# Performance work log

Hardware: AMD Instinct MI355X
Metric: run time of the kernel (lower is better)

## Reference

```python
import jax, jax.numpy as jnp
import numpy as np

M, K, N = 2048, 4096, 8192
BITS = 4
GROUP_SIZE = 128
G = K // GROUP_SIZE  # 32 groups
PACK = 8 // BITS     # 2 values per int8 byte


def setup_inputs() -> dict:
    key = jax.random.key(0)
    k_a, k_q, k_s = jax.random.split(key, 3)
    A = jax.random.normal(k_a, (M, K), dtype=jnp.float16)
    # packed 4-bit weights: each byte stores two uint4 values (low nibble first)
    qweight = jax.random.randint(k_q, (N, K // PACK), 0, 256, dtype=jnp.int32)
    scales = jax.random.normal(k_s, (N, G), dtype=jnp.float16)
    zeros = jnp.zeros((N, G), dtype=jnp.float16)
    bias = jnp.zeros((N,), dtype=jnp.float16)
    return {"A": A, "qweight": qweight, "scales": scales, "zeros": zeros, "bias": bias}


def _dequantize(qweight, scales, zeros):
    # unpack two uint4 values per byte (low nibble is the earlier element)
    q = qweight.astype(jnp.int32)
    lo = q & 0xF
    hi = (q >> 4) & 0xF
    intw = jnp.stack([lo, hi], axis=-1).reshape(N, K)  # [N, K] uint4 values
    # zeros_mode='original': w = (q - zero) * scale, per group of GROUP_SIZE
    wq = intw.reshape(N, G, GROUP_SIZE).astype(jnp.float16)
    w = (wq - zeros[:, :, None]) * scales[:, :, None]
    return w.reshape(N, K)


def reference(A, qweight, scales, zeros, bias):
    W = _dequantize(qweight, scales, zeros)          # [N, K] fp16
    out = jnp.einsum('mk,nk->mn', A, W) + bias       # 'nt' layout: A @ W^T + bias
    return out.astype(A.dtype)
```

## Files before the change

kernel.cpp:

```cpp
#include <hip/hip_runtime.h>
#include <stdint.h>

#define MDIM 2048
#define KDIM 4096
#define NDIM 8192
#define NG   32
#define QROW 2048
#define NT2  64
#define LSTR 36
#define BUFH 32768

typedef __attribute__((ext_vector_type(4))) float    f32x4;
typedef __attribute__((ext_vector_type(2))) _Float16 f16x2;
typedef __attribute__((ext_vector_type(8))) _Float16 f16x8;
typedef __attribute__((ext_vector_type(4))) int      i32x4;

#define CVT2(a,b) __builtin_bit_cast(f16x2, __builtin_amdgcn_cvt_pkrtz((a),(b)))
#define BCU(x)    __builtin_bit_cast(unsigned, (x))
#define BCH2(x)   __builtin_bit_cast(f16x2, (x))
#define MFMA16(A,B,C) __builtin_amdgcn_mfma_f32_16x16x32_f16((A),(B),(C),0,0,0)
#define LDSREAD(DST, OFF) __builtin_memcpy(&(DST), &lds[(OFF)], 16)

__device__ __forceinline__ void gload_lds16(const void* g, void* l) {
  __builtin_amdgcn_global_load_lds(
      (const __attribute__((address_space(1))) void*)g,
      (__attribute__((address_space(3))) void*)l, 16, 0, 0);
}

__device__ __forceinline__ uint4 dequant8(i32x4 q, float sf, float zf) {
  const _Float16 sh = (_Float16)sf;
  const _Float16 bh = (_Float16)(-zf * sf);
  const f16x2 s2 = {sh, sh}, b2 = {bh, bh};
  const f16x2 k2 = {(_Float16)1024.0f, (_Float16)1024.0f};
  uint4 r;
#define DQE(QV, DST) do {                                                   \
    unsigned Bb_ = (unsigned)(QV) & 0xFFu;                                  \
    unsigned bits_ = ((Bb_ | (Bb_ << 12)) & 0x000F000Fu) | 0x64006400u;     \
    DST = BCU((f16x2)((BCH2(bits_) - k2) * s2 + b2));                       \
  } while (0)
  DQE(q.x, r.x); DQE(q.y, r.y); DQE(q.z, r.z); DQE(q.w, r.w);
#undef DQE
  return r;
}

__global__ __launch_bounds__(256) void dequant_w_kernel(
    const int* __restrict__ qw, const float* __restrict__ scales,
    const float* __restrict__ zeros, _Float16* __restrict__ Wf)
{
  const size_t total = (size_t)NDIM * (KDIM / 8);
  for (size_t t = (size_t)blockIdx.x * blockDim.x + threadIdx.x; t < total;
       t += (size_t)gridDim.x * blockDim.x) {
    i32x4 q;
    __builtin_memcpy(&q, qw + 4 * t, 16);
    const int n = (int)(t >> 9);
    const int k = (int)((t & 511) << 3);
    const int g = k >> 7;
    uint4 w = dequant8(q, scales[n * NG + g], zeros[n * NG + g]);
    __builtin_memcpy(Wf + (size_t)n * KDIM + k, &w, 16);
  }
}

__global__ __launch_bounds__(256) void conv_a_kernel(
    const float* __restrict__ A, _Float16* __restrict__ Af)
{
  const size_t total = (size_t)MDIM * (KDIM / 8);
  for (size_t t = (size_t)blockIdx.x * blockDim.x + threadIdx.x; t < total;
       t += (size_t)gridDim.x * blockDim.x) {
    f32x4 v0, v1;
    __builtin_memcpy(&v0, A + 8 * t,     16);
    __builtin_memcpy(&v1, A + 8 * t + 4, 16);
    uint4 h;
    h.x = BCU(CVT2(v0.x, v0.y));
    h.y = BCU(CVT2(v0.z, v0.w));
    h.z = BCU(CVT2(v1.x, v1.y));
    h.w = BCU(CVT2(v1.z, v1.w));
    __builtin_memcpy(Af + 8 * t, &h, 16);
  }
}

__global__ __launch_bounds__(512) void gemm_f16_kernel(
    const _Float16* __restrict__ Af,
    const _Float16* __restrict__ Wf,
    const float* __restrict__ bias,
    float* __restrict__ out)
{
  __shared__ __align__(16) _Float16 lds[2 * BUFH];

  const int tid  = threadIdx.x;
  const int wave = tid >> 6;
  const int lane = tid & 63;
  const int n0 = blockIdx.x << 8;
  const int m0 = blockIdx.y << 8;
  const int wm = (wave >> 2) << 7;
  const int wn = (wave & 3) << 6;

  f32x4 acc[8][4] = {};

  const int srow   = tid >> 3;
  const int schunk = (tid & 7) ^ ((tid >> 3) & 7);
  const _Float16* aU0 = Af + (size_t)(m0 + srow) * KDIM + schunk * 8;
  const _Float16* aU1 = aU0 + (size_t)64 * KDIM;
  const _Float16* aU2 = aU0 + (size_t)128 * KDIM;
  const _Float16* aU3 = aU0 + (size_t)192 * KDIM;
  const _Float16* bU0 = Wf + (size_t)(n0 + srow) * KDIM + schunk * 8;
  const _Float16* bU1 = bU0 + (size_t)64 * KDIM;
  const _Float16* bU2 = bU0 + (size_t)128 * KDIM;
  const _Float16* bU3 = bU0 + (size_t)192 * KDIM;

#define ISSUE(T) do {                                                  \
    _Float16* d_ = &lds[((T) & 1) * BUFH + (wave << 9)];               \
    const size_t ko_ = (size_t)(T) << 6;                               \
    gload_lds16(aU0 + ko_, d_);                                        \
    gload_lds16(aU1 + ko_, d_ + 4096);                                 \
    gload_lds16(aU2 + ko_, d_ + 8192);                                 \
    gload_lds16(aU3 + ko_, d_ + 12288);                                \
    gload_lds16(bU0 + ko_, d_ + 16384);                                \
    gload_lds16(bU1 + ko_, d_ + 20480);                                \
    gload_lds16(bU2 + ko_, d_ + 24576);                                \
    gload_lds16(bU3 + ko_, d_ + 28672);                                \
  } while (0)

  const int fr = lane & 15;
  const int h4 = lane >> 4;
  const int ck0 = (((0 + h4) ^ (fr & 7))) << 3;
  const int ck1 = (((4 + h4) ^ (fr & 7))) << 3;
  int raOff[8], rbOff[4];
#pragma unroll
  for (int i = 0; i < 8; ++i) raOff[i] = (wm + 16 * i + fr) * 64;
#pragma unroll
  for (int j = 0; j < 4; ++j) rbOff[j] = 16384 + (wn + 16 * j + fr) * 64;

#define COMPUTE(T) do {                                                \
    const int bb_ = ((T) & 1) * BUFH;                                  \
    f16x8 b0_[4], b1_[4];                                              \
    _Pragma("unroll")                                                  \
    for (int j = 0; j < 4; ++j) {                                      \
      LDSREAD(b0_[j], bb_ + rbOff[j] + ck0);                           \
      LDSREAD(b1_[j], bb_ + rbOff[j] + ck1);                           \
    }                                                                  \
    _Pragma("unroll")                                                  \
    for (int i = 0; i < 8; ++i) {                                      \
      f16x8 a0_, a1_;                                                  \
      LDSREAD(a0_, bb_ + raOff[i] + ck0);                              \
      LDSREAD(a1_, bb_ + raOff[i] + ck1);                              \
      _Pragma("unroll")                                                \
      for (int j = 0; j < 4; ++j)                                      \
        acc[i][j] = MFMA16(a0_, b0_[j], acc[i][j]);                    \
      _Pragma("unroll")                                                \
      for (int j = 0; j < 4; ++j)                                      \
        acc[i][j] = MFMA16(a1_, b1_[j], acc[i][j]);                    \
    }                                                                  \
  } while (0)

#define PH_MFMA(R) do {                                                \
    __builtin_amdgcn_s_setprio(1);                                     \
    _Pragma("unroll")                                                  \
    for (int j = 0; j < 4; ++j) {                                      \
      acc[(R)][j]     = MFMA16(aA0, bf0[j], acc[(R)][j]);              \
      acc[(R) + 1][j] = MFMA16(aB0, bf0[j], acc[(R) + 1][j]);          \
    }                                                                  \
    _Pragma("unroll")                                                  \
    for (int j = 0; j < 4; ++j) {                                      \
      acc[(R)][j]     = MFMA16(aA1, bf1[j], acc[(R)][j]);              \
      acc[(R) + 1][j] = MFMA16(aB1, bf1[j], acc[(R) + 1][j]);          \
    }                                                                  \
    __builtin_amdgcn_s_setprio(0);                                     \
  } while (0)

  ISSUE(0); ISSUE(1);

#pragma clang loop unroll(disable)
  for (int t = 0; t < NT2 - 2; ++t) {
    asm volatile("s_waitcnt vmcnt(8)" ::: "memory");
    __builtin_amdgcn_s_barrier();
    const int bb = (t & 1) * BUFH;

    f16x8 bf0[4], bf1[4], aA0, aA1, aB0, aB1;

#pragma unroll
    for (int j = 0; j < 4; ++j) {
      LDSREAD(bf0[j], bb + rbOff[j] + ck0);
      LDSREAD(bf1[j], bb + rbOff[j] + ck1);
    }
    LDSREAD(aA0, bb + raOff[0] + ck0);
    LDSREAD(aA1, bb + raOff[0] + ck1);
    LDSREAD(aB0, bb + raOff[1] + ck0);
    LDSREAD(aB1, bb + raOff[1] + ck1);
    __builtin_amdgcn_s_barrier();
    PH_MFMA(0);

    LDSREAD(aA0, bb + raOff[2] + ck0);
    LDSREAD(aA1, bb + raOff[2] + ck1);
    LDSREAD(aB0, bb + raOff[3] + ck0);
    LDSREAD(aB1, bb + raOff[3] + ck1);
    __builtin_amdgcn_s_barrier();
    PH_MFMA(2);

    LDSREAD(aA0, bb + raOff[4] + ck0);
    LDSREAD(aA1, bb + raOff[4] + ck1);
    LDSREAD(aB0, bb + raOff[5] + ck0);
    LDSREAD(aB1, bb + raOff[5] + ck1);
    __builtin_amdgcn_s_barrier();
    PH_MFMA(4);

    LDSREAD(aA0, bb + raOff[6] + ck0);
    LDSREAD(aA1, bb + raOff[6] + ck1);
    LDSREAD(aB0, bb + raOff[7] + ck0);
    LDSREAD(aB1, bb + raOff[7] + ck1);
    __builtin_amdgcn_s_barrier();
    ISSUE(t + 2);
    PH_MFMA(6);
  }

  asm volatile("s_waitcnt vmcnt(8)" ::: "memory");
  __builtin_amdgcn_s_barrier();
  COMPUTE(NT2 - 2);
  asm volatile("s_waitcnt vmcnt(0)" ::: "memory");
  __builtin_amdgcn_s_barrier();
  COMPUTE(NT2 - 1);

#undef ISSUE
#undef COMPUTE
#undef PH_MFMA

  const int cr = (lane >> 4) << 2;
  const int cc = lane & 15;
#pragma unroll
  for (int j = 0; j < 4; ++j) {
    const int n = n0 + wn + j * 16 + cc;
    const float bv = bias[n];
#pragma unroll
    for (int i = 0; i < 8; ++i) {
      const int mrow = m0 + wm + i * 16 + cr;
#pragma unroll
      for (int r = 0; r < 4; ++r)
        out[(size_t)(mrow + r) * NDIM + n] = acc[i][j][r] + bv;
    }
  }
}

__global__ __launch_bounds__(256, 4) void qlin_fused_kernel(
    const float* __restrict__ A, const int* __restrict__ qw,
    const float* __restrict__ scales, const float* __restrict__ zeros,
    const float* __restrict__ bias, float* __restrict__ out)
{
  __shared__ _Float16 As[2][128 * LSTR];
  __shared__ _Float16 Bs[2][128 * LSTR];

  const int tid  = threadIdx.x;
  const int wave = tid >> 6;
  const int lane = tid & 63;
  const int n0 = blockIdx.x << 7;
  const int m0 = blockIdx.y << 7;
  const int wm = (wave >> 1) << 6;
  const int wn = (wave & 1) << 6;

  f32x4 acc[4][4] = {};

  const int r4 = tid >> 2;
  const int c4 = tid & 3;

  const float* aP0 = A + (size_t)(m0 + r4) * KDIM + c4 * 8;
  const float* aP1 = aP0 + (size_t)64 * KDIM;
  const int*   qP0 = qw + (size_t)(n0 + r4) * QROW + c4 * 4;
  const int*   qP1 = qP0 + (size_t)64 * QROW;
  const float* sP0 = scales + (size_t)(n0 + r4) * NG;
  const float* zP0 = zeros  + (size_t)(n0 + r4) * NG;
  const float* sP1 = sP0 + (size_t)64 * NG;
  const float* zP1 = zP0 + (size_t)64 * NG;

  const int aD0 = r4 * LSTR + c4 * 8;
  const int aD1 = (r4 + 64) * LSTR + c4 * 8;

  const int fr = lane & 15;
  const int k0 = (lane >> 4) * 8;
  const int ra0 = (wm +  0 + fr) * LSTR + k0;
  const int ra1 = (wm + 16 + fr) * LSTR + k0;
  const int ra2 = (wm + 32 + fr) * LSTR + k0;
  const int ra3 = (wm + 48 + fr) * LSTR + k0;
  const int rb0 = (wn +  0 + fr) * LSTR + k0;
  const int rb1 = (wn + 16 + fr) * LSTR + k0;
  const int rb2 = (wn + 32 + fr) * LSTR + k0;
  const int rb3 = (wn + 48 + fr) * LSTR + k0;

  f32x4 pa0, pa1, pa2, pa3;
  i32x4 pq0, pq1;
  float psf0, pzf0, psf1, pzf1;

#define ISSUE(KT) do {                                                        \
    __builtin_memcpy(&pa0, aP0 + (size_t)(KT) * 32,     16);                  \
    __builtin_memcpy(&pa1, aP0 + (size_t)(KT) * 32 + 4, 16);                  \
    __builtin_memcpy(&pa2, aP1 + (size_t)(KT) * 32,     16);                  \
    __builtin_memcpy(&pa3, aP1 + (size_t)(KT) * 32 + 4, 16);                  \
    __builtin_memcpy(&pq0, qP0 + (size_t)(KT) * 16, 16);                      \
    __builtin_memcpy(&pq1, qP1 + (size_t)(KT) * 16, 16);                      \
    const int g_ = (KT) >> 2;                                                 \
    psf0 = sP0[g_]; pzf0 = zP0[g_];                                           \
    psf1 = sP1[g_]; pzf1 = zP1[g_];                                           \
  } while (0)

#define STAGE(P) do {                                                         \
    uint4 aw0_;                                                               \
    aw0_.x = BCU(CVT2(pa0.x, pa0.y));                                         \
    aw0_.y = BCU(CVT2(pa0.z, pa0.w));                                         \
    aw0_.z = BCU(CVT2(pa1.x, pa1.y));                                         \
    aw0_.w = BCU(CVT2(pa1.z, pa1.w));                                         \
    __builtin_memcpy(&As[P][aD0], &aw0_, 16);                                 \
    uint4 aw1_;                                                               \
    aw1_.x = BCU(CVT2(pa2.x, pa2.y));                                         \
    aw1_.y = BCU(CVT2(pa2.z, pa2.w));                                         \
    aw1_.z = BCU(CVT2(pa3.x, pa3.y));                                         \
    aw1_.w = BCU(CVT2(pa3.z, pa3.w));                                         \
    __builtin_memcpy(&As[P][aD1], &aw1_, 16);                                 \
    uint4 bw0_ = dequant8(pq0, psf0, pzf0);                                   \
    __builtin_memcpy(&Bs[P][aD0], &bw0_, 16);                                 \
    uint4 bw1_ = dequant8(pq1, psf1, pzf1);                                   \
    __builtin_memcpy(&Bs[P][aD1], &bw1_, 16);                                 \
  } while (0)

#define COMPUTE(P) do {                                                       \
    f16x8 af[4], bfr[4];                                                      \
    __builtin_memcpy(&af[0], &As[P][ra0], 16);                                \
    __builtin_memcpy(&af[1], &As[P][ra1], 16);                                \
    __builtin_memcpy(&af[2], &As[P][ra2], 16);                                \
    __builtin_memcpy(&af[3], &As[P][ra3], 16);                                \
    __builtin_memcpy(&bfr[0], &Bs[P][rb0], 16);                               \
    __builtin_memcpy(&bfr[1], &Bs[P][rb1], 16);                               \
    __builtin_memcpy(&bfr[2], &Bs[P][rb2], 16);                               \
    __builtin_memcpy(&bfr[3], &Bs[P][rb3], 16);                               \
    _Pragma("unroll")                                                         \
    for (int i = 0; i < 4; ++i)                                               \
      _Pragma("unroll")                                                       \
      for (int j = 0; j < 4; ++j)                                             \
        acc[i][j] = MFMA16(af[i], bfr[j], acc[i][j]);                         \
  } while (0)

  ISSUE(0);
  STAGE(0);
  __syncthreads();

#pragma clang loop unroll(disable)
  for (int kt = 0; kt < 127; ++kt) {
    const int p = kt & 1;
    ISSUE(kt + 1);
    COMPUTE(p);
    STAGE(p ^ 1);
    __syncthreads();
  }
  COMPUTE(1);

#undef ISSUE
#undef STAGE
#undef COMPUTE

  const int cr = (lane >> 4) << 2;
  const int cc = lane & 15;
#pragma unroll
  for (int j = 0; j < 4; ++j) {
    const int n = n0 + wn + j * 16 + cc;
    const float bv = bias[n];
#pragma unroll
    for (int i = 0; i < 4; ++i) {
      const int mrow = m0 + wm + i * 16 + cr;
#pragma unroll
      for (int r = 0; r < 4; ++r)
        out[(size_t)(mrow + r) * NDIM + n] = acc[i][j][r] + bv;
    }
  }
}

extern "C" void kernel_launch(void* const* d_in, const int* in_sizes, int n_in,
                              void* d_out, int out_size, void* d_ws, size_t ws_size,
                              hipStream_t stream) {
  const float* A      = (const float*)d_in[0];
  const int*   qwp    = (const int*)d_in[1];
  const float* scales = (const float*)d_in[2];
  const float* zerosp = (const float*)d_in[3];
  const float* biasp  = (const float*)d_in[4];
  float*       outp   = (float*)d_out;

  const size_t needW = (size_t)NDIM * KDIM * sizeof(_Float16);
  const size_t needA = (size_t)MDIM * KDIM * sizeof(_Float16);

  if (ws_size >= needW + needA) {
    _Float16* Wf = (_Float16*)d_ws;
    _Float16* Af = (_Float16*)((char*)d_ws + needW);
    dequant_w_kernel<<<2048, 256, 0, stream>>>(qwp, scales, zerosp, Wf);
    conv_a_kernel<<<2048, 256, 0, stream>>>(A, Af);
    dim3 grid(NDIM / 256, MDIM / 256);
    gemm_f16_kernel<<<grid, 512, 0, stream>>>(Af, Wf, biasp, outp);
  } else {
    dim3 grid(NDIM / 128, MDIM / 128);
    qlin_fused_kernel<<<grid, 256, 0, stream>>>(A, qwp, scales, zerosp, biasp, outp);
  }
}
```

Before: 159.4 us.

## Switch f16 GEMM inner loop from 16x16x32 to 32x32x16 MFMA tiles

Replaces the 16x16x32 MFMA instructions with 32x32x16 MFMA, regrouping each wave's 128x64 tile into 4x2 blocks of 32x32 with 16-float accumulators. The LDS fragment reads, swizzled chunk offsets, phased barrier schedule and output store mapping are rewritten to match the new operand and accumulator layout. The larger instruction reuses each operand over more outputs, so fewer LDS reads and instructions are needed per FLOP. In exchange there are more K-steps per tile and a different pipeline phase balance with one A row block per phase.

```diff
diff --git a/kernel.cpp b/kernel.cpp
--- a/kernel.cpp
+++ b/kernel.cpp
@@ -10,15 +10,17 @@
 #define LSTR 36
 #define BUFH 32768
 
-typedef __attribute__((ext_vector_type(4))) float    f32x4;
-typedef __attribute__((ext_vector_type(2))) _Float16 f16x2;
-typedef __attribute__((ext_vector_type(8))) _Float16 f16x8;
-typedef __attribute__((ext_vector_type(4))) int      i32x4;
+typedef __attribute__((ext_vector_type(4)))  float    f32x4;
+typedef __attribute__((ext_vector_type(16))) float    f32x16;
+typedef __attribute__((ext_vector_type(2)))  _Float16 f16x2;
+typedef __attribute__((ext_vector_type(8)))  _Float16 f16x8;
+typedef __attribute__((ext_vector_type(4)))  int      i32x4;
 
 #define CVT2(a,b) __builtin_bit_cast(f16x2, __builtin_amdgcn_cvt_pkrtz((a),(b)))
 #define BCU(x)    __builtin_bit_cast(unsigned, (x))
 #define BCH2(x)   __builtin_bit_cast(f16x2, (x))
 #define MFMA16(A,B,C) __builtin_amdgcn_mfma_f32_16x16x32_f16((A),(B),(C),0,0,0)
+#define MFMA32(A,B,C) __builtin_amdgcn_mfma_f32_32x32x16_f16((A),(B),(C),0,0,0)
 #define LDSREAD(DST, OFF) __builtin_memcpy(&(DST), &lds[(OFF)], 16)
 
 __device__ __forceinline__ void gload_lds16(const void* g, void* l) {
@@ -94,7 +96,7 @@
   const int wm = (wave >> 2) << 7;
   const int wn = (wave & 3) << 6;
 
-  f32x4 acc[8][4] = {};
+  f32x16 acc[4][2] = {};
 
   const int srow   = tid >> 3;
   const int schunk = (tid & 7) ^ ((tid >> 3) & 7);
@@ -120,52 +122,55 @@
     gload_lds16(bU3 + ko_, d_ + 28672);                                \
   } while (0)
 
-  const int fr = lane & 15;
-  const int h4 = lane >> 4;
-  const int ck0 = (((0 + h4) ^ (fr & 7))) << 3;
-  const int ck1 = (((4 + h4) ^ (fr & 7))) << 3;
-  int raOff[8], rbOff[4];
-#pragma unroll
-  for (int i = 0; i < 8; ++i) raOff[i] = (wm + 16 * i + fr) * 64;
-#pragma unroll
-  for (int j = 0; j < 4; ++j) rbOff[j] = 16384 + (wn + 16 * j + fr) * 64;
+  const int fr32 = lane & 31;
+  const int h2   = lane >> 5;
+  const int sw8  = fr32 & 7;
+  int raOff[4], rbOff[2], ckk[4];
+#pragma unroll
+  for (int i = 0; i < 4; ++i) raOff[i] = (wm + 32 * i + fr32) * 64;
+#pragma unroll
+  for (int j = 0; j < 2; ++j) rbOff[j] = 16384 + (wn + 32 * j + fr32) * 64;
+#pragma unroll
+  for (int ks = 0; ks < 4; ++ks) ckk[ks] = ((2 * ks + h2) ^ sw8) << 3;
 
 #define COMPUTE(T) do {                                                \
     const int bb_ = ((T) & 1) * BUFH;                                  \
-    f16x8 b0_[4], b1_[4];                                              \
+    f16x8 b_[2][4];                                                    \
     _Pragma("unroll")                                                  \
-    for (int j = 0; j < 4; ++j) {                                      \
-      LDSREAD(b0_[j], bb_ + rbOff[j] + ck0);                           \
-      LDSREAD(b1_[j], bb_ + rbOff[j] + ck1);                           \
+    for (int j = 0; j < 2; ++j)                                        \
+      _Pragma("unroll")                                                \
+      for (int ks = 0; ks < 4; ++ks)                                   \
+        LDSREAD(b_[j][ks], bb_ + rbOff[j] + ckk[ks]);                  \
+    _Pragma("unroll")                                                  \
+    for (int i = 0; i < 4; ++i) {                                      \
+      _Pragma("unroll")                                                \
+      for (int ks = 0; ks < 4; ++ks) {                                 \
+        f16x8 a_;                                                      \
+        LDSREAD(a_, bb_ + raOff[i] + ckk[ks]);                         \
+        acc[i][0] = MFMA32(a_, b_[0][ks], acc[i][0]);                  \
+        acc[i][1] = MFMA32(a_, b_[1][ks], acc[i][1]);                  \
+      }                                                                \
     }                                                                  \
-    _Pragma("unroll")                                                  \
-    for (int i = 0; i < 8; ++i) {                                      \
-      f16x8 a0_, a1_;                                                  \
-      LDSREAD(a0_, bb_ + raOff[i] + ck0);                              \
-      LDSREAD(a1_, bb_ + raOff[i] + ck1);                              \
-      _Pragma("unroll")                                                \
-      for (int j = 0; j < 4; ++j)                                      \
-        acc[i][j] = MFMA16(a0_, b0_[j], acc[i][j]);                    \
-      _Pragma("unroll")                                                \
-      for (int j = 0; j < 4; ++j)                                      \
-        acc[i][j] = MFMA16(a1_, b1_[j], acc[i][j]);                    \
-    }                                                                  \
-  } while (0)
-
-#define PH_MFMA(R) do {                                                \
+  } while (0)
+
+#define PH_MFMA(I) do {                                                \
     __builtin_amdgcn_s_setprio(1);                                     \
-    _Pragma("unroll")                                                  \
-    for (int j = 0; j < 4; ++j) {                                      \
-      acc[(R)][j]     = MFMA16(aA0, bf0[j], acc[(R)][j]);              \
-      acc[(R) + 1][j] = MFMA16(aB0, bf0[j], acc[(R) + 1][j]);          \
-    }                                                                  \
-    _Pragma("unroll")                                                  \
-    for (int j = 0; j < 4; ++j) {                                      \
-      acc[(R)][j]     = MFMA16(aA1, bf1[j], acc[(R)][j]);              \
-      acc[(R) + 1][j] = MFMA16(aB1, bf1[j], acc[(R) + 1][j]);          \
-    }                                                                  \
+    acc[I][0] = MFMA32(aK0, bf[0][0], acc[I][0]);                      \
+    acc[I][1] = MFMA32(aK0, bf[1][0], acc[I][1]);                      \
+    acc[I][0] = MFMA32(aK1, bf[0][1], acc[I][0]);                      \
+    acc[I][1] = MFMA32(aK1, bf[1][1], acc[I][1]);                      \
+    acc[I][0] = MFMA32(aK2, bf[0][2], acc[I][0]);                      \
+    acc[I][1] = MFMA32(aK2, bf[1][2], acc[I][1]);                      \
+    acc[I][0] = MFMA32(aK3, bf[0][3], acc[I][0]);                      \
+    acc[I][1] = MFMA32(aK3, bf[1][3], acc[I][1]);                      \
     __builtin_amdgcn_s_setprio(0);                                     \
   } while (0)
+
+#define RD_A(I)                                                        \
+    LDSREAD(aK0, bb + raOff[I] + ckk[0]);                              \
+    LDSREAD(aK1, bb + raOff[I] + ckk[1]);                              \
+    LDSREAD(aK2, bb + raOff[I] + ckk[2]);                              \
+    LDSREAD(aK3, bb + raOff[I] + ckk[3]);
 
   ISSUE(0); ISSUE(1);
 
@@ -175,41 +180,29 @@
     __builtin_amdgcn_s_barrier();
     const int bb = (t & 1) * BUFH;
 
-    f16x8 bf0[4], bf1[4], aA0, aA1, aB0, aB1;
-
-#pragma unroll
-    for (int j = 0; j < 4; ++j) {
-      LDSREAD(bf0[j], bb + rbOff[j] + ck0);
-      LDSREAD(bf1[j], bb + rbOff[j] + ck1);
-    }
-    LDSREAD(aA0, bb + raOff[0] + ck0);
-    LDSREAD(aA1, bb + raOff[0] + ck1);
-    LDSREAD(aB0, bb + raOff[1] + ck0);
-    LDSREAD(aB1, bb + raOff[1] + ck1);
+    f16x8 bf[2][4], aK0, aK1, aK2, aK3;
+
+#pragma unroll
+    for (int j = 0; j < 2; ++j)
+#pragma unroll
+      for (int ks = 0; ks < 4; ++ks)
+        LDSREAD(bf[j][ks], bb + rbOff[j] + ckk[ks]);
+    RD_A(0)
     __builtin_amdgcn_s_barrier();
     PH_MFMA(0);
 
-    LDSREAD(aA0, bb + raOff[2] + ck0);
-    LDSREAD(aA1, bb + raOff[2] + ck1);
-    LDSREAD(aB0, bb + raOff[3] + ck0);
-    LDSREAD(aB1, bb + raOff[3] + ck1);
+    RD_A(1)
+    __builtin_amdgcn_s_barrier();
+    PH_MFMA(1);
+
+    RD_A(2)
     __builtin_amdgcn_s_barrier();
     PH_MFMA(2);
 
-    LDSREAD(aA0, bb + raOff[4] + ck0);
-    LDSREAD(aA1, bb + raOff[4] + ck1);
-    LDSREAD(aB0, bb + raOff[5] + ck0);
-    LDSREAD(aB1, bb + raOff[5] + ck1);
-    __builtin_amdgcn_s_barrier();
-    PH_MFMA(4);
-
-    LDSREAD(aA0, bb + raOff[6] + ck0);
-    LDSREAD(aA1, bb + raOff[6] + ck1);
-    LDSREAD(aB0, bb + raOff[7] + ck0);
-    LDSREAD(aB1, bb + raOff[7] + ck1);
+    RD_A(3)
     __builtin_amdgcn_s_barrier();
     ISSUE(t + 2);
-    PH_MFMA(6);
+    PH_MFMA(3);
   }
 
   asm volatile("s_waitcnt vmcnt(8)" ::: "memory");
@@ -222,19 +215,21 @@
 #undef ISSUE
 #undef COMPUTE
 #undef PH_MFMA
-
-  const int cr = (lane >> 4) << 2;
-  const int cc = lane & 15;
-#pragma unroll
-  for (int j = 0; j < 4; ++j) {
-    const int n = n0 + wn + j * 16 + cc;
-    const float bv = bias[n];
-#pragma unroll
-    for (int i = 0; i < 8; ++i) {
-      const int mrow = m0 + wm + i * 16 + cr;
-#pragma unroll
-      for (int r = 0; r < 4; ++r)
-        out[(size_t)(mrow + r) * NDIM + n] = acc[i][j][r] + bv;
+#undef RD_A
+
+  const int cc = lane & 31;
+  const int rbase = 4 * (lane >> 5);
+#pragma unroll
+  for (int i = 0; i < 4; ++i) {
+#pragma unroll
+    for (int j = 0; j < 2; ++j) {
+      const int n = n0 + wn + 32 * j + cc;
+      const float bv = bias[n];
+#pragma unroll
+      for (int reg = 0; reg < 16; ++reg) {
+        const int mrow = m0 + wm + 32 * i + (reg & 3) + 8 * (reg >> 2) + rbase;
+        out[(size_t)mrow * NDIM + n] = acc[i][j][reg] + bv;
+      }
     }
   }
 }
```

Result: slower. 177.5 us (+11.3%).

## Split next-tile global-to-LDS loads into four parts interleaved across MFMA phases

Applied to the files above, without the earlier changes.

The single burst of eight global-to-LDS loads per K-step is split into four two-load stages. Stage 1 of tile t+2 is issued at the end of the iteration, and stages 2 to 4 of tile t+1 are issued between the MFMA phases. The loop-top wait is relaxed to vmcnt(2), and each phase now ends with a barrier plus an lgkmcnt(0) wait and a scheduling barrier. The aim is to spread memory traffic evenly across the compute phases. In exchange, most of the tile is now prefetched less than one iteration ahead, which can expose load latency, and the extra waits and barriers add synchronisation overhead.

```diff
diff --git a/kernel.cpp b/kernel.cpp
--- a/kernel.cpp
+++ b/kernel.cpp
@@ -107,15 +107,27 @@
   const _Float16* bU2 = bU0 + (size_t)128 * KDIM;
   const _Float16* bU3 = bU0 + (size_t)192 * KDIM;
 
-#define ISSUE(T) do {                                                  \
-    _Float16* d_ = &lds[((T) & 1) * BUFH + (wave << 9)];               \
-    const size_t ko_ = (size_t)(T) << 6;                               \
+#define STAGE_P1(X) do {                                               \
+    _Float16* d_ = &lds[((X) & 1) * BUFH + (wave << 9)];               \
+    const size_t ko_ = (size_t)(X) << 6;                               \
     gload_lds16(aU0 + ko_, d_);                                        \
     gload_lds16(aU1 + ko_, d_ + 4096);                                 \
+  } while (0)
+#define STAGE_P2(X) do {                                               \
+    _Float16* d_ = &lds[((X) & 1) * BUFH + (wave << 9)];               \
+    const size_t ko_ = (size_t)(X) << 6;                               \
     gload_lds16(aU2 + ko_, d_ + 8192);                                 \
     gload_lds16(aU3 + ko_, d_ + 12288);                                \
+  } while (0)
+#define STAGE_P3(X) do {                                               \
+    _Float16* d_ = &lds[((X) & 1) * BUFH + (wave << 9)];               \
+    const size_t ko_ = (size_t)(X) << 6;                               \
     gload_lds16(bU0 + ko_, d_ + 16384);                                \
     gload_lds16(bU1 + ko_, d_ + 20480);                                \
+  } while (0)
+#define STAGE_P4(X) do {                                               \
+    _Float16* d_ = &lds[((X) & 1) * BUFH + (wave << 9)];               \
+    const size_t ko_ = (size_t)(X) << 6;                               \
     gload_lds16(bU2 + ko_, d_ + 24576);                                \
     gload_lds16(bU3 + ko_, d_ + 28672);                                \
   } while (0)
@@ -167,11 +179,23 @@
     __builtin_amdgcn_s_setprio(0);                                     \
   } while (0)
 
-  ISSUE(0); ISSUE(1);
+#define RD_A(I)                                                        \
+    LDSREAD(aA0, bb + raOff[I] + ck0);                                 \
+    LDSREAD(aA1, bb + raOff[I] + ck1);                                 \
+    LDSREAD(aB0, bb + raOff[(I) + 1] + ck0);                           \
+    LDSREAD(aB1, bb + raOff[(I) + 1] + ck1);
+
+#define MIDSYNC                                                        \
+    __builtin_amdgcn_s_barrier();                                      \
+    asm volatile("s_waitcnt lgkmcnt(0)" ::: "memory");                 \
+    __builtin_amdgcn_sched_barrier(0);
+
+  STAGE_P1(0); STAGE_P2(0); STAGE_P3(0); STAGE_P4(0);
+  STAGE_P1(1);
 
 #pragma clang loop unroll(disable)
   for (int t = 0; t < NT2 - 2; ++t) {
-    asm volatile("s_waitcnt vmcnt(8)" ::: "memory");
+    asm volatile("s_waitcnt vmcnt(2)" ::: "memory");
     __builtin_amdgcn_s_barrier();
     const int bb = (t & 1) * BUFH;
 
@@ -182,36 +206,31 @@
       LDSREAD(bf0[j], bb + rbOff[j] + ck0);
       LDSREAD(bf1[j], bb + rbOff[j] + ck1);
     }
-    LDSREAD(aA0, bb + raOff[0] + ck0);
-    LDSREAD(aA1, bb + raOff[0] + ck1);
-    LDSREAD(aB0, bb + raOff[1] + ck0);
-    LDSREAD(aB1, bb + raOff[1] + ck1);
+    RD_A(0)
+    STAGE_P2(t + 1);
+    MIDSYNC
+    PH_MFMA(0);
     __builtin_amdgcn_s_barrier();
-    PH_MFMA(0);
-
-    LDSREAD(aA0, bb + raOff[2] + ck0);
-    LDSREAD(aA1, bb + raOff[2] + ck1);
-    LDSREAD(aB0, bb + raOff[3] + ck0);
-    LDSREAD(aB1, bb + raOff[3] + ck1);
+
+    RD_A(2)
+    STAGE_P3(t + 1);
+    MIDSYNC
+    PH_MFMA(2);
     __builtin_amdgcn_s_barrier();
-    PH_MFMA(2);
-
-    LDSREAD(aA0, bb + raOff[4] + ck0);
-    LDSREAD(aA1, bb + raOff[4] + ck1);
-    LDSREAD(aB0, bb + raOff[5] + ck0);
-    LDSREAD(aB1, bb + raOff[5] + ck1);
+
+    RD_A(4)
+    STAGE_P4(t + 1);
+    MIDSYNC
+    PH_MFMA(4);
     __builtin_amdgcn_s_barrier();
-    PH_MFMA(4);
-
-    LDSREAD(aA0, bb + raOff[6] + ck0);
-    LDSREAD(aA1, bb + raOff[6] + ck1);
-    LDSREAD(aB0, bb + raOff[7] + ck0);
-    LDSREAD(aB1, bb + raOff[7] + ck1);
-    __builtin_amdgcn_s_barrier();
-    ISSUE(t + 2);
+
+    RD_A(6)
+    MIDSYNC
+    STAGE_P1(t + 2);
     PH_MFMA(6);
   }
 
+  STAGE_P2(NT2 - 1); STAGE_P3(NT2 - 1); STAGE_P4(NT2 - 1);
   asm volatile("s_waitcnt vmcnt(8)" ::: "memory");
   __builtin_amdgcn_s_barrier();
   COMPUTE(NT2 - 2);
@@ -219,9 +238,14 @@
   __builtin_amdgcn_s_barrier();
   COMPUTE(NT2 - 1);
 
-#undef ISSUE
+#undef STAGE_P1
+#undef STAGE_P2
+#undef STAGE_P3
+#undef STAGE_P4
 #undef COMPUTE
 #undef PH_MFMA
+#undef RD_A
+#undef MIDSYNC
 
   const int cr = (lane >> 4) << 2;
   const int cc = lane & 15;
```

Result: faster. 155.6 us (-2.4%).
